# Kernel tuning notes

Measured on AMD Instinct MI355X. Metric: run time of the kernel, lower is better.

The kernel has to match this reference:

```python
import jax, jax.numpy as jnp
import numpy as np

D_MODEL = 1024
NUM_HEADS = 16
D_K = D_MODEL // NUM_HEADS
ROPE_THETA = 10000.0


def apply_rope(x, pos):
    # x: [B, H, S, d_k], pos: [S] int
    half = x.shape[-1] // 2
    inv_freq = ROPE_THETA ** (-jnp.arange(half, dtype=jnp.float32) * 2.0 / x.shape[-1])
    ang = pos.astype(jnp.float32)[:, None] * inv_freq[None, :]  # [S, half]
    cos, sin = jnp.cos(ang), jnp.sin(ang)
    x1 = x[..., 0::2]
    x2 = x[..., 1::2]
    r1 = x1 * cos - x2 * sin
    r2 = x1 * sin + x2 * cos
    return jnp.stack([r1, r2], axis=-1).reshape(x.shape)


def setup_inputs() -> dict:
    key = jax.random.key(0)
    ks = jax.random.split(key, 5)
    B, S = 4, 2048
    scale = 1.0 / np.sqrt(D_MODEL)
    x = jax.random.normal(ks[0], (B, S, D_MODEL), dtype=jnp.float32)
    w_q = jax.random.normal(ks[1], (D_MODEL, D_MODEL), dtype=jnp.float32) * scale
    w_k = jax.random.normal(ks[2], (D_MODEL, D_MODEL), dtype=jnp.float32) * scale
    w_v = jax.random.normal(ks[3], (D_MODEL, D_MODEL), dtype=jnp.float32) * scale
    w_o = jax.random.normal(ks[4], (D_MODEL, D_MODEL), dtype=jnp.float32) * scale
    token_positions = jnp.arange(S, dtype=jnp.int32)
    return {"x": x, "w_q": w_q, "w_k": w_k, "w_v": w_v, "w_o": w_o, "token_positions": token_positions}


def reference(x, w_q, w_k, w_v, w_o, token_positions):
    B, S, _ = x.shape
    def proj(w):
        return (x @ w.T).reshape(B, S, NUM_HEADS, D_K).transpose(0, 2, 1, 3)  # [B,H,S,d_k]
    q, k, v = proj(w_q), proj(w_k), proj(w_v)
    q = apply_rope(q, token_positions)
    k = apply_rope(k, token_positions)
    logits = jnp.einsum('bhid,bhjd->bhij', q, k) / jnp.sqrt(jnp.float32(D_K))
    causal = jnp.tril(jnp.ones((S, S), dtype=bool))
    logits = jnp.where(causal[None, None], logits, -jnp.inf)
    weights = jax.nn.softmax(logits, axis=-1)
    attn = jnp.einsum('bhij,bhjd->bhid', weights, v)  # [B,H,S,d_k]
    attn = attn.transpose(0, 2, 1, 3).reshape(B, S, D_MODEL)
    return attn @ w_o.T
```

## Files before the change

kernel.cpp:

```cpp
#include <hip/hip_runtime.h>
#include <hip/hip_bf16.h>
#include <stdint.h>

#define DM   1024
#define SEQ  2048
#define BATCH 4
#define NH   16
#define DK   64
#define NTK  16

typedef __attribute__((ext_vector_type(8))) __bf16 bf16x8;
typedef __attribute__((ext_vector_type(4))) float f32x4;
typedef __attribute__((ext_vector_type(4))) unsigned short ushort4_t;
typedef __attribute__((ext_vector_type(4))) unsigned int uint4_t;

typedef __attribute__((address_space(1))) const unsigned int GU32;
typedef __attribute__((address_space(3))) unsigned int LU32;

__device__ inline void gl_lds16(const void* g, void* l) {
  __builtin_amdgcn_global_load_lds((GU32*)g, (LU32*)l, 16, 0, 0);
}

__device__ inline f32x4 mfma16(bf16x8 a, bf16x8 b, f32x4 c) {
  return __builtin_amdgcn_mfma_f32_16x16x32_bf16(a, b, c, 0, 0, 0);
}

__device__ inline unsigned short f2bf(float f) {
  unsigned u = __float_as_uint(f);
  u += 0x7fffu + ((u >> 16) & 1u);
  return (unsigned short)(u >> 16);
}

__device__ inline unsigned cvt_pk_bf16(float a, float b) {
  unsigned r;
  asm("v_cvt_pk_bf16_f32 %0, %1, %2" : "=v"(r) : "v"(a), "v"(b));
  return r;
}

__device__ inline float fexp2(float x) {
  float r;
  asm("v_exp_f32 %0, %1" : "=v"(r) : "v"(x));
  return r;
}

__device__ inline int swz_of(int r) { return ((r & 6) << 2) | ((r & 1) << 5); }
__device__ inline int bswz(int r) { return ((r & 6) << 3) | ((r & 1) << 6); }

__global__ void prep_kernel(const float* __restrict__ x,
                            const float* __restrict__ wq, const float* __restrict__ wk,
                            const float* __restrict__ wv, const float* __restrict__ wo,
                            const int* __restrict__ tp,
                            unsigned short* __restrict__ xbf,
                            unsigned short* __restrict__ wbf,
                            float2* __restrict__ tab)
{
  const int NX4 = (BATCH*SEQ*DM)/4;
  const int NW4 = (DM*DM)/4;
  int idx = blockIdx.x*256 + threadIdx.x;
  if (idx < NX4) {
    float4 v = ((const float4*)x)[idx];
    ushort4_t o; o[0]=f2bf(v.x); o[1]=f2bf(v.y); o[2]=f2bf(v.z); o[3]=f2bf(v.w);
    ((ushort4_t*)xbf)[idx] = o;
  } else if (idx < NX4 + 4*NW4) {
    int t = idx - NX4;
    int wsel = t >> 18;
    int off = t & (NW4-1);
    const float* src = (wsel==0) ? wq : (wsel==1) ? wk : (wsel==2) ? wv : wo;
    float4 v = ((const float4*)src)[off];
    ushort4_t o; o[0]=f2bf(v.x); o[1]=f2bf(v.y); o[2]=f2bf(v.z); o[3]=f2bf(v.w);
    ((ushort4_t*)wbf)[wsel*NW4 + off] = o;
  } else {
    int t = idx - NX4 - 4*NW4;
    if (t < SEQ*32) {
      int s = t >> 5, i = t & 31;
      float invf = exp2f(-(float)i * (13.287712379549449f/32.0f));
      float ang = (float)tp[s] * invf;
      float sn, cs; sincosf(ang, &sn, &cs);
      tab[t] = make_float2(cs, sn);
    }
  }
}

template<int MODE>
__global__ __launch_bounds__(256, 2)
void gemm_db(const unsigned short* __restrict__ A,
             const unsigned short* __restrict__ Wall,
             unsigned short* __restrict__ qbf,
             unsigned short* __restrict__ kbf,
             unsigned short* __restrict__ vt,
             float* __restrict__ ofp,
             const float2* __restrict__ tab)
{
  __shared__ __align__(16) char lds[65536];
  const int tid = threadIdx.x;
  const int bid = blockIdx.x;
  int sel, mt, nt;
  if (MODE == 0) {
    sel = bid >> 9;
    int r = bid & 511;
    int xcd = r & 7, idx = r >> 3;
    mt = xcd*8 + (idx >> 3);  nt = idx & 7;
  } else {
    sel = 3;
    int xcd = bid & 7, idx = bid >> 3;
    mt = xcd*8 + (idx >> 3);  nt = idx & 7;
  }
  const unsigned short* Bm = Wall + (size_t)sel*DM*DM;
  const int a0 = mt*128, b0r = nt*128;
  const int w = tid>>6, lane = tid&63, ln = lane&15, g = lane>>4;
  const int wm = (w>>1)*64, wn = (w&1)*64;

  const char* src[8];
  {
    int rr = tid >> 3;
    int c  = (tid & 7) * 8;
    #pragma unroll
    for (int i = 0; i < 4; ++i) {
      int r_ = i*32 + rr;
      int cs = c ^ swz_of(r_);
      src[i]   = (const char*)(A  + (size_t)(a0  + r_)*DM + cs);
      src[i+4] = (const char*)(Bm + (size_t)(b0r + r_)*DM + cs);
    }
  }

  int offA[4], offB[4];
  #pragma unroll
  for (int m = 0; m < 4; ++m) {
    int R  = wm + m*16 + ln;
    offA[m] = R*128 + ((g*8 ^ swz_of(R)) * 2);
    int Rb = wn + m*16 + ln;
    offB[m] = 16384 + Rb*128 + ((g*8 ^ swz_of(Rb)) * 2);
  }

  f32x4 acc[4][4];
  #pragma unroll
  for (int i=0;i<4;i++)
    #pragma unroll
    for (int j=0;j<4;j++) acc[i][j] = (f32x4){0.f,0.f,0.f,0.f};

  #pragma unroll
  for (int i = 0; i < 8; ++i) gl_lds16(src[i],       lds +         i*4096 + tid*16);
  #pragma unroll
  for (int i = 0; i < 8; ++i) gl_lds16(src[i] + 128, lds + 32768 + i*4096 + tid*16);

  for (int t = 0; t < NTK; ++t) {
    char* sb = lds + (t & 1) * 32768;
    if (t < NTK-1) asm volatile("s_waitcnt vmcnt(8)" ::: "memory");
    else           asm volatile("s_waitcnt vmcnt(0)" ::: "memory");
    __builtin_amdgcn_sched_barrier(0);
    __builtin_amdgcn_s_barrier();
    asm volatile("" ::: "memory");
    __builtin_amdgcn_sched_barrier(0);

    bf16x8 fa[4][2], fb[4][2];
    #pragma unroll
    for (int m = 0; m < 4; ++m) {
      fa[m][0] = *(const bf16x8*)(sb + offA[m]);
      fa[m][1] = *(const bf16x8*)(sb + (offA[m] ^ 64));
      fb[m][0] = *(const bf16x8*)(sb + offB[m]);
      fb[m][1] = *(const bf16x8*)(sb + (offB[m] ^ 64));
    }
    asm volatile("s_waitcnt lgkmcnt(0)" ::: "memory");
    __builtin_amdgcn_sched_barrier(0);
    __builtin_amdgcn_s_barrier();
    asm volatile("" ::: "memory");
    __builtin_amdgcn_sched_barrier(0);

    if (t + 2 < NTK) {
      const int kb = (t + 2) * 128;
      #pragma unroll
      for (int i = 0; i < 8; ++i)
        gl_lds16(src[i] + kb, sb + i*4096 + tid*16);
    }
    __builtin_amdgcn_s_setprio(1);
    #pragma unroll
    for (int h = 0; h < 2; ++h)
      #pragma unroll
      for (int m = 0; m < 4; ++m)
        #pragma unroll
        for (int n = 0; n < 4; ++n)
          acc[m][n] = mfma16(fa[m][h], fb[n][h], acc[m][n]);
    __builtin_amdgcn_s_setprio(0);
  }

  if (MODE == 1) {
    #pragma unroll
    for (int i=0;i<4;i++) {
      int m = a0 + wm + i*16 + g*4;
      #pragma unroll
      for (int jn=0;jn<4;jn++) {
        int n = b0r + wn + jn*16 + ln;
        #pragma unroll
        for (int j=0;j<4;j++)
          ofp[(size_t)(m+j)*DM + n] = acc[i][jn][j];
      }
    }
  } else if (sel == 2) {
    #pragma unroll
    for (int i=0;i<4;i++) {
      int m0 = a0 + wm + i*16 + g*4;
      int bb = m0>>11, s0 = m0&2047;
      #pragma unroll
      for (int jn=0;jn<4;jn++) {
        int n = b0r + wn + jn*16 + ln;
        int h = n>>6, d = n&63;
        ushort4_t o4;
        #pragma unroll
        for (int j=0;j<4;j++) o4[j] = f2bf(acc[i][jn][j]);
        *(ushort4_t*)&vt[(((size_t)bb*NH + h)*DK + d)*SEQ + s0] = o4;
      }
    }
  } else {
    unsigned short* dst = sel ? kbf : qbf;
    const float qs = sel ? 1.0f : 0.1803368802f;
    #pragma unroll
    for (int jn=0;jn<4;jn++) {
      int n = b0r + wn + jn*16 + ln;
      int h = n>>6, d = n&63, di = d>>1, par = d&1;
      #pragma unroll
      for (int i=0;i<4;i++) {
        #pragma unroll
        for (int j=0;j<4;j++) {
          int m = a0 + wm + i*16 + g*4 + j;
          int bb = m>>11, s = m&2047;
          float v = acc[i][jn][j];
          float pv = __shfl_xor(v, 1);
          float2 cssn = tab[s*32 + di];
          float r = par ? (v*cssn.x + pv*cssn.y) : (v*cssn.x - pv*cssn.y);
          dst[((size_t)(bb*NH + h)*SEQ + s)*DK + d] = f2bf(r*qs);
        }
      }
    }
  }
}

__global__ __launch_bounds__(128, 2)
void attn_fa(const unsigned short* __restrict__ qbf,
             const unsigned short* __restrict__ kbf,
             const unsigned short* __restrict__ vtg,
             unsigned short* __restrict__ attnbf)
{
  __shared__ __align__(16) char kv_lds[32768];
  __shared__ __align__(16) char pl_lds[4096];
  const int bh = blockIdx.x, pr = blockIdx.y;
  const int qbA = 31 - pr;
  const int NTa = qbA + 1;
  const int NTtot = 33;
  const int tid = threadIdx.x, w = tid>>6, lane = tid&63, ln = lane&15, g = lane>>4;
  const int bb = bh>>4, h = bh&15;

  uint4_t ov = {0x3F803F80u, 0x3F803F80u, 0x3F803F80u, 0x3F803F80u};
  const bf16x8 ones = *(bf16x8*)&ov;

  const int rr = tid >> 3;
  const int cb = (tid & 7) * 16;
  const char* ks[4]; const char* vs[4];
  #pragma unroll
  for (int i = 0; i < 4; ++i) {
    int row = rr + i*16;
    ks[i] = (const char*)(kbf + ((size_t)bh*SEQ + row)*DK) + (cb ^ bswz(row));
    vs[i] = (const char*)(vtg + ((size_t)bh*DK  + row)*SEQ) + (cb ^ bswz(row));
  }

  const int ok0 = (g*16) ^ bswz(ln);
  char* plw = pl_lds + w*2048 + ln*128;
  const int plswz = (ln & 7) << 4;

  #pragma unroll
  for (int i = 0; i < 4; ++i) {
    gl_lds16(ks[i], kv_lds + i*2048 + tid*16);
    gl_lds16(vs[i], kv_lds + 8192 + i*2048 + tid*16);
  }
  #pragma unroll
  for (int i = 0; i < 4; ++i) {
    gl_lds16(ks[i] + 8192, kv_lds + 16384 + i*2048 + tid*16);
    gl_lds16(vs[i] + 128,  kv_lds + 16384 + 8192 + i*2048 + tid*16);
  }

  int q0a = qbA*64 + w*32;
  int q0b = q0a + 16;
  const unsigned short* qrA = qbf + ((size_t)bh*SEQ + q0a + ln)*DK;
  const unsigned short* qrB = qbf + ((size_t)bh*SEQ + q0b + ln)*DK;
  bf16x8 qa0 = *(const bf16x8*)(qrA + g*8);
  bf16x8 qa1 = *(const bf16x8*)(qrA + 32 + g*8);
  bf16x8 qb0 = *(const bf16x8*)(qrB + g*8);
  bf16x8 qb1 = *(const bf16x8*)(qrB + 32 + g*8);

  f32x4 oA[4], oB[4], osA, osB;
  #pragma unroll
  for (int f=0;f<4;f++) { oA[f] = (f32x4){0,0,0,0}; oB[f] = (f32x4){0,0,0,0}; }
  osA = (f32x4){0,0,0,0}; osB = (f32x4){0,0,0,0};

  for (int u = 0; u < NTtot; ++u) {
    const int tloc  = (u < NTa) ? u : u - NTa;
    const int NTcur = (u < NTa) ? NTa : NTtot - NTa;
    char* sb = kv_lds + (u & 1) * 16384;
    if (u < NTtot-1) asm volatile("s_waitcnt vmcnt(8)" ::: "memory");
    else             asm volatile("s_waitcnt vmcnt(0)" ::: "memory");
    __builtin_amdgcn_sched_barrier(0);
    __builtin_amdgcn_s_barrier();
    asm volatile("" ::: "memory");
    __builtin_amdgcn_sched_barrier(0);

    bf16x8 kf[4][2], vfr[4][2];
    #pragma unroll
    for (int a=0;a<4;a++) {
      kf[a][0]  = *(const bf16x8*)(sb + a*2048 + (ok0 ^  0) + ln*128);
      kf[a][1]  = *(const bf16x8*)(sb + a*2048 + (ok0 ^ 64) + ln*128);
      vfr[a][0] = *(const bf16x8*)(sb + 8192 + a*2048 + (ok0 ^  0) + ln*128);
      vfr[a][1] = *(const bf16x8*)(sb + 8192 + a*2048 + (ok0 ^ 64) + ln*128);
    }
    asm volatile("s_waitcnt lgkmcnt(0)" ::: "memory");
    __builtin_amdgcn_sched_barrier(0);
    __builtin_amdgcn_s_barrier();
    asm volatile("" ::: "memory");
    __builtin_amdgcn_sched_barrier(0);

    if (u + 2 < NTtot) {
      const int t2 = (u + 2 < NTa) ? u + 2 : u + 2 - NTa;
      const size_t kO = (size_t)t2*8192, vO = (size_t)t2*128;
      #pragma unroll
      for (int i = 0; i < 4; ++i) {
        gl_lds16(ks[i] + kO, sb + i*2048 + tid*16);
        gl_lds16(vs[i] + vO, sb + 8192 + i*2048 + tid*16);
      }
    }

    if (u == NTa) {
      #pragma unroll
      for (int j=0;j<4;j++) {
        float liA = 1.0f / osA[j];
        float liB = 1.0f / osB[j];
        int sA = q0a + g*4 + j, sB = q0b + g*4 + j;
        #pragma unroll
        for (int f=0;f<4;f++) {
          attnbf[((size_t)bb*SEQ + sA)*DM + h*DK + f*16 + ln] = f2bf(oA[f][j]*liA);
          attnbf[((size_t)bb*SEQ + sB)*DM + h*DK + f*16 + ln] = f2bf(oB[f][j]*liB);
        }
      }
      q0a = pr*64 + w*32;
      q0b = q0a + 16;
      const unsigned short* qa = qbf + ((size_t)bh*SEQ + q0a + ln)*DK;
      const unsigned short* qb = qbf + ((size_t)bh*SEQ + q0b + ln)*DK;
      qa0 = *(const bf16x8*)(qa + g*8);
      qa1 = *(const bf16x8*)(qa + 32 + g*8);
      qb0 = *(const bf16x8*)(qb + g*8);
      qb1 = *(const bf16x8*)(qb + 32 + g*8);
      #pragma unroll
      for (int f=0;f<4;f++) { oA[f] = (f32x4){0,0,0,0}; oB[f] = (f32x4){0,0,0,0}; }
      osA = (f32x4){0,0,0,0}; osB = (f32x4){0,0,0,0};
    }

    f32x4 saA[4], saB[4];
    __builtin_amdgcn_s_setprio(1);
    #pragma unroll
    for (int kvf=0;kvf<4;kvf++) {
      f32x4 za = (f32x4){0,0,0,0};
      za = mfma16(kf[kvf][0], qa0, za);
      za = mfma16(kf[kvf][1], qa1, za);
      saA[kvf] = za;
      f32x4 zb = (f32x4){0,0,0,0};
      zb = mfma16(kf[kvf][0], qb0, zb);
      zb = mfma16(kf[kvf][1], qb1, zb);
      saB[kvf] = zb;
    }
    __builtin_amdgcn_s_setprio(0);

    const bool diag = (tloc == NTcur-1);

    {
      if (diag) {
        int thr = q0a + ln - tloc*64 - g*4;
        #pragma unroll
        for (int kvf=0;kvf<4;kvf++)
          #pragma unroll
          for (int j=0;j<4;j++)
            if (kvf*16 + j > thr) saA[kvf][j] = -1e30f;
      }
      #pragma unroll
      for (int kvf=0;kvf<4;kvf++) {
        float p0 = fexp2(saA[kvf][0]);
        float p1 = fexp2(saA[kvf][1]);
        float p2 = fexp2(saA[kvf][2]);
        float p3 = fexp2(saA[kvf][3]);
        uint2 pk;
        pk.x = cvt_pk_bf16(p0, p1);
        pk.y = cvt_pk_bf16(p2, p3);
        *(uint2*)(plw + ((kvf*32 + g*8) ^ plswz)) = pk;
      }
      asm volatile("s_waitcnt lgkmcnt(0)" ::: "memory");
      __builtin_amdgcn_sched_barrier(0);
      #pragma unroll
      for (int c=0;c<2;c++) {
        bf16x8 pfA = *(const bf16x8*)(plw + ((c*64 + g*16) ^ plswz));
        #pragma unroll
        for (int f=0;f<4;f++)
          oA[f] = mfma16(pfA, vfr[f][c], oA[f]);
        osA = mfma16(pfA, ones, osA);
      }
    }

    {
      if (diag) {
        int thr = q0b + ln - tloc*64 - g*4;
        #pragma unroll
        for (int kvf=0;kvf<4;kvf++)
          #pragma unroll
          for (int j=0;j<4;j++)
            if (kvf*16 + j > thr) saB[kvf][j] = -1e30f;
      }
      #pragma unroll
      for (int kvf=0;kvf<4;kvf++) {
        float p0 = fexp2(saB[kvf][0]);
        float p1 = fexp2(saB[kvf][1]);
        float p2 = fexp2(saB[kvf][2]);
        float p3 = fexp2(saB[kvf][3]);
        uint2 pk;
        pk.x = cvt_pk_bf16(p0, p1);
        pk.y = cvt_pk_bf16(p2, p3);
        *(uint2*)(plw + ((kvf*32 + g*8) ^ plswz)) = pk;
      }
      asm volatile("s_waitcnt lgkmcnt(0)" ::: "memory");
      __builtin_amdgcn_sched_barrier(0);
      __builtin_amdgcn_s_setprio(1);
      #pragma unroll
      for (int c=0;c<2;c++) {
        bf16x8 pfB = *(const bf16x8*)(plw + ((c*64 + g*16) ^ plswz));
        #pragma unroll
        for (int f=0;f<4;f++)
          oB[f] = mfma16(pfB, vfr[f][c], oB[f]);
        osB = mfma16(pfB, ones, osB);
      }
      __builtin_amdgcn_s_setprio(0);
    }
  }

  #pragma unroll
  for (int j=0;j<4;j++) {
    float liA = 1.0f / osA[j];
    float liB = 1.0f / osB[j];
    int sA = q0a + g*4 + j, sB = q0b + g*4 + j;
    #pragma unroll
    for (int f=0;f<4;f++) {
      attnbf[((size_t)bb*SEQ + sA)*DM + h*DK + f*16 + ln] = f2bf(oA[f][j]*liA);
      attnbf[((size_t)bb*SEQ + sB)*DM + h*DK + f*16 + ln] = f2bf(oB[f][j]*liB);
    }
  }
}

extern "C" void kernel_launch(void* const* d_in, const int* in_sizes, int n_in,
                              void* d_out, int out_size, void* d_ws, size_t ws_size,
                              hipStream_t stream)
{
  const float* x  = (const float*)d_in[0];
  const float* wq = (const float*)d_in[1];
  const float* wk = (const float*)d_in[2];
  const float* wv = (const float*)d_in[3];
  const float* wo = (const float*)d_in[4];
  const int*   tp = (const int*)d_in[5];

  const size_t XB = (size_t)BATCH*SEQ*DM*2;
  const size_t WB = (size_t)DM*DM*2;

  char* ws = (char*)d_ws;
  unsigned short* xbf = (unsigned short*)(ws);
  unsigned short* qbf = (unsigned short*)(ws + XB);
  unsigned short* kbf = (unsigned short*)(ws + 2*XB);
  unsigned short* vt  = (unsigned short*)(ws + 3*XB);
  unsigned short* abf = (unsigned short*)(ws + 4*XB);
  unsigned short* wbf = (unsigned short*)(ws + 5*XB);
  float2* tab = (float2*)(ws + 5*XB + 4*WB);

  prep_kernel<<<12544, 256, 0, stream>>>(x, wq, wk, wv, wo, tp, xbf, wbf, tab);

  gemm_db<0><<<1536, 256, 0, stream>>>(xbf, wbf, qbf, kbf, vt, nullptr, tab);
  attn_fa<<<dim3(64,16), 128, 0, stream>>>(qbf, kbf, vt, abf);
  gemm_db<1><<<512, 256, 0, stream>>>(abf, wbf, nullptr, nullptr, nullptr,
                                      (float*)d_out, nullptr);
}
```

Before: 162.9 us.

## Replace QKV projection GEMM with 256x256-tile, 8-wave pipelined kernel

The QKV projection moves from 128x128 tiles with 4 waves to a new kernel using 256x256 tiles, 512 threads and a 128KB LDS double buffer. Each k-step is split into four quarter-stage loads interleaved with MFMA sub-blocks, so global-to-LDS traffic overlaps compute and operand reuse per tile goes up. The costs are 384 blocks that may not fill all CUs evenly, heavy register pressure from 32 accumulators per thread, and lower occupancy. The output GEMM keeps the old kernel, cut down to its output-projection mode, and the barrier sequences are folded into macros.

```diff
diff --git a/kernel.cpp b/kernel.cpp
--- a/kernel.cpp
+++ b/kernel.cpp
@@ -45,6 +45,15 @@
 
 __device__ inline int swz_of(int r) { return ((r & 6) << 2) | ((r & 1) << 5); }
 __device__ inline int bswz(int r) { return ((r & 6) << 3) | ((r & 1) << 6); }
+
+#define BAR_SYNC() do { \
+  __builtin_amdgcn_sched_barrier(0); \
+  __builtin_amdgcn_s_barrier(); \
+  asm volatile("" ::: "memory"); \
+  __builtin_amdgcn_sched_barrier(0); } while(0)
+#define LGKM0() do { \
+  asm volatile("s_waitcnt lgkmcnt(0)" ::: "memory"); \
+  __builtin_amdgcn_sched_barrier(0); } while(0)
 
 __global__ void prep_kernel(const float* __restrict__ x,
                             const float* __restrict__ wq, const float* __restrict__ wk,
@@ -81,31 +90,188 @@
   }
 }
 
+__global__ __launch_bounds__(512, 2)
+void gemm8(const unsigned short* __restrict__ A,
+           const unsigned short* __restrict__ Wall,
+           unsigned short* __restrict__ qbf,
+           unsigned short* __restrict__ kbf,
+           unsigned short* __restrict__ vt,
+           const float2* __restrict__ tab)
+{
+  __shared__ __align__(16) char lds[131072];
+  const int tid = threadIdx.x;
+  const int bid = blockIdx.x;
+  const int sel = bid >> 7;
+  const int rb = bid & 127;
+  const int xcd = rb & 7, idx = rb >> 3;
+  const int mt = xcd*4 + (idx>>2), nt = idx & 3;
+  const unsigned short* Bw = Wall + (size_t)sel*DM*DM;
+  const int a0 = mt*256, b0 = nt*256;
+  const int w = tid>>6, lane = tid&63, ln = lane&15, g = lane>>4;
+  const int wm = (w>>2)*128, wn = (w&3)*64;
+
+  const int r0 = tid >> 3;
+  const int csw = ((tid & 7) * 16) ^ bswz(r0);
+  const char* pA = (const char*)A  + ((size_t)(a0 + r0))*2048 + csw;
+  const char* pB = (const char*)Bw + ((size_t)(b0 + r0))*2048 + csw;
+
+  auto stage = [&](int hh) {
+    int T = hh>>2, j = hh&3;
+    const char* s = ((j<2) ? pB : pA) + (size_t)(j&1)*262144 + (size_t)T*128;
+    char* d = lds + (T&1)*65536 + ((j<2) ? (32768 + j*16384) : ((j-2)*16384))
+              + tid*16;
+    gl_lds16(s,          d);
+    gl_lds16(s + 131072, d + 8192);
+  };
+
+  const int swz = bswz(ln);
+  const int arow = (wm + ln)*128;
+  const int brow = 32768 + (wn + ln)*128;
+
+  f32x4 acc[8][4];
+  #pragma unroll
+  for (int i=0;i<8;i++)
+    #pragma unroll
+    for (int j=0;j<4;j++) acc[i][j] = (f32x4){0.f,0.f,0.f,0.f};
+
+  #pragma unroll
+  for (int hh = 0; hh < 6; ++hh) stage(hh);
+  asm volatile("s_waitcnt vmcnt(4)" ::: "memory");
+  BAR_SYNC();
+
+  int hptr = 6;
+  for (int U = 0; U < 16; ++U) {
+    char* sb = lds + (U&1)*65536;
+    bf16x8 Afr[4][2], Bfr[4][2];
+
+    #pragma unroll
+    for (int mi=0;mi<4;++mi)
+      #pragma unroll
+      for (int kh=0;kh<2;++kh)
+        Afr[mi][kh] = *(const bf16x8*)(sb + arow + mi*2048 + (((kh<<6)|(g<<4)) ^ swz));
+    #pragma unroll
+    for (int nf=0;nf<2;++nf)
+      #pragma unroll
+      for (int kh=0;kh<2;++kh)
+        Bfr[nf][kh] = *(const bf16x8*)(sb + brow + nf*2048 + (((kh<<6)|(g<<4)) ^ swz));
+    if (hptr < 64) stage(hptr++);
+    BAR_SYNC();
+    LGKM0();
+    __builtin_amdgcn_s_setprio(1);
+    #pragma unroll
+    for (int mi=0;mi<4;++mi)
+      #pragma unroll
+      for (int nf=0;nf<2;++nf)
+        #pragma unroll
+        for (int kh=0;kh<2;++kh)
+          acc[mi][nf] = mfma16(Afr[mi][kh], Bfr[nf][kh], acc[mi][nf]);
+    __builtin_amdgcn_s_setprio(0);
+    BAR_SYNC();
+
+    #pragma unroll
+    for (int nf=2;nf<4;++nf)
+      #pragma unroll
+      for (int kh=0;kh<2;++kh)
+        Bfr[nf][kh] = *(const bf16x8*)(sb + brow + nf*2048 + (((kh<<6)|(g<<4)) ^ swz));
+    if (hptr < 64) stage(hptr++);
+    BAR_SYNC();
+    LGKM0();
+    __builtin_amdgcn_s_setprio(1);
+    #pragma unroll
+    for (int mi=0;mi<4;++mi)
+      #pragma unroll
+      for (int nf=2;nf<4;++nf)
+        #pragma unroll
+        for (int kh=0;kh<2;++kh)
+          acc[mi][nf] = mfma16(Afr[mi][kh], Bfr[nf][kh], acc[mi][nf]);
+    __builtin_amdgcn_s_setprio(0);
+    BAR_SYNC();
+
+    #pragma unroll
+    for (int mi=0;mi<4;++mi)
+      #pragma unroll
+      for (int kh=0;kh<2;++kh)
+        Afr[mi][kh] = *(const bf16x8*)(sb + arow + 8192 + mi*2048 + (((kh<<6)|(g<<4)) ^ swz));
+    if (hptr < 64) stage(hptr++);
+    BAR_SYNC();
+    LGKM0();
+    __builtin_amdgcn_s_setprio(1);
+    #pragma unroll
+    for (int mi=0;mi<4;++mi)
+      #pragma unroll
+      for (int nf=0;nf<2;++nf)
+        #pragma unroll
+        for (int kh=0;kh<2;++kh)
+          acc[4+mi][nf] = mfma16(Afr[mi][kh], Bfr[nf][kh], acc[4+mi][nf]);
+    __builtin_amdgcn_s_setprio(0);
+    BAR_SYNC();
+
+    if (hptr < 64) stage(hptr++);
+    __builtin_amdgcn_s_setprio(1);
+    #pragma unroll
+    for (int mi=0;mi<4;++mi)
+      #pragma unroll
+      for (int nf=2;nf<4;++nf)
+        #pragma unroll
+        for (int kh=0;kh<2;++kh)
+          acc[4+mi][nf] = mfma16(Afr[mi][kh], Bfr[nf][kh], acc[4+mi][nf]);
+    __builtin_amdgcn_s_setprio(0);
+    if (U < 14)       asm volatile("s_waitcnt vmcnt(4)" ::: "memory");
+    else if (U == 14) asm volatile("s_waitcnt vmcnt(0)" ::: "memory");
+    BAR_SYNC();
+  }
+
+  if (sel == 2) {
+    #pragma unroll
+    for (int mi=0;mi<8;++mi) {
+      int m0 = a0 + wm + mi*16 + g*4;
+      int bb = m0>>11, s0 = m0&2047;
+      #pragma unroll
+      for (int nf=0;nf<4;++nf) {
+        int n = b0 + wn + nf*16 + ln;
+        int h = n>>6, d = n&63;
+        ushort4_t o4;
+        #pragma unroll
+        for (int jj=0;jj<4;++jj) o4[jj] = f2bf(acc[mi][nf][jj]);
+        *(ushort4_t*)&vt[(((size_t)bb*NH + h)*DK + d)*SEQ + s0] = o4;
+      }
+    }
+  } else {
+    unsigned short* dst = sel ? kbf : qbf;
+    const float qs = sel ? 1.0f : 0.1803368802f;
+    #pragma unroll
+    for (int nf=0;nf<4;++nf) {
+      int n = b0 + wn + nf*16 + ln;
+      int h = n>>6, d = n&63, di = d>>1, par = d&1;
+      #pragma unroll
+      for (int mi=0;mi<8;++mi) {
+        #pragma unroll
+        for (int jj=0;jj<4;++jj) {
+          int m = a0 + wm + mi*16 + g*4 + jj;
+          int bb = m>>11, s = m&2047;
+          float v = acc[mi][nf][jj];
+          float pv = __shfl_xor(v, 1);
+          float2 cssn = tab[s*32 + di];
+          float r = par ? (v*cssn.x + pv*cssn.y) : (v*cssn.x - pv*cssn.y);
+          dst[((size_t)(bb*NH + h)*SEQ + s)*DK + d] = f2bf(r*qs);
+        }
+      }
+    }
+  }
+}
+
 template<int MODE>
 __global__ __launch_bounds__(256, 2)
 void gemm_db(const unsigned short* __restrict__ A,
              const unsigned short* __restrict__ Wall,
-             unsigned short* __restrict__ qbf,
-             unsigned short* __restrict__ kbf,
-             unsigned short* __restrict__ vt,
-             float* __restrict__ ofp,
-             const float2* __restrict__ tab)
+             float* __restrict__ ofp)
 {
   __shared__ __align__(16) char lds[65536];
   const int tid = threadIdx.x;
   const int bid = blockIdx.x;
-  int sel, mt, nt;
-  if (MODE == 0) {
-    sel = bid >> 9;
-    int r = bid & 511;
-    int xcd = r & 7, idx = r >> 3;
-    mt = xcd*8 + (idx >> 3);  nt = idx & 7;
-  } else {
-    sel = 3;
-    int xcd = bid & 7, idx = bid >> 3;
-    mt = xcd*8 + (idx >> 3);  nt = idx & 7;
-  }
-  const unsigned short* Bm = Wall + (size_t)sel*DM*DM;
+  int xcd = bid & 7, idx = bid >> 3;
+  int mt = xcd*8 + (idx >> 3), nt = idx & 7;
+  const unsigned short* Bm = Wall + (size_t)3*DM*DM;
   const int a0 = mt*128, b0r = nt*128;
   const int w = tid>>6, lane = tid&63, ln = lane&15, g = lane>>4;
   const int wm = (w>>1)*64, wn = (w&1)*64;
@@ -147,10 +313,7 @@
     char* sb = lds + (t & 1) * 32768;
     if (t < NTK-1) asm volatile("s_waitcnt vmcnt(8)" ::: "memory");
     else           asm volatile("s_waitcnt vmcnt(0)" ::: "memory");
-    __builtin_amdgcn_sched_barrier(0);
-    __builtin_amdgcn_s_barrier();
-    asm volatile("" ::: "memory");
-    __builtin_amdgcn_sched_barrier(0);
+    BAR_SYNC();
 
     bf16x8 fa[4][2], fb[4][2];
     #pragma unroll
@@ -160,11 +323,8 @@
       fb[m][0] = *(const bf16x8*)(sb + offB[m]);
       fb[m][1] = *(const bf16x8*)(sb + (offB[m] ^ 64));
     }
-    asm volatile("s_waitcnt lgkmcnt(0)" ::: "memory");
-    __builtin_amdgcn_sched_barrier(0);
-    __builtin_amdgcn_s_barrier();
-    asm volatile("" ::: "memory");
-    __builtin_amdgcn_sched_barrier(0);
+    LGKM0();
+    BAR_SYNC();
 
     if (t + 2 < NTK) {
       const int kb = (t + 2) * 128;
@@ -183,53 +343,15 @@
     __builtin_amdgcn_s_setprio(0);
   }
 
-  if (MODE == 1) {
-    #pragma unroll
-    for (int i=0;i<4;i++) {
-      int m = a0 + wm + i*16 + g*4;
-      #pragma unroll
-      for (int jn=0;jn<4;jn++) {
-        int n = b0r + wn + jn*16 + ln;
-        #pragma unroll
-        for (int j=0;j<4;j++)
-          ofp[(size_t)(m+j)*DM + n] = acc[i][jn][j];
-      }
-    }
-  } else if (sel == 2) {
-    #pragma unroll
-    for (int i=0;i<4;i++) {
-      int m0 = a0 + wm + i*16 + g*4;
-      int bb = m0>>11, s0 = m0&2047;
-      #pragma unroll
-      for (int jn=0;jn<4;jn++) {
-        int n = b0r + wn + jn*16 + ln;
-        int h = n>>6, d = n&63;
-        ushort4_t o4;
-        #pragma unroll
-        for (int j=0;j<4;j++) o4[j] = f2bf(acc[i][jn][j]);
-        *(ushort4_t*)&vt[(((size_t)bb*NH + h)*DK + d)*SEQ + s0] = o4;
-      }
-    }
-  } else {
-    unsigned short* dst = sel ? kbf : qbf;
-    const float qs = sel ? 1.0f : 0.1803368802f;
+  #pragma unroll
+  for (int i=0;i<4;i++) {
+    int m = a0 + wm + i*16 + g*4;
     #pragma unroll
     for (int jn=0;jn<4;jn++) {
       int n = b0r + wn + jn*16 + ln;
-      int h = n>>6, d = n&63, di = d>>1, par = d&1;
-      #pragma unroll
-      for (int i=0;i<4;i++) {
-        #pragma unroll
-        for (int j=0;j<4;j++) {
-          int m = a0 + wm + i*16 + g*4 + j;
-          int bb = m>>11, s = m&2047;
-          float v = acc[i][jn][j];
-          float pv = __shfl_xor(v, 1);
-          float2 cssn = tab[s*32 + di];
-          float r = par ? (v*cssn.x + pv*cssn.y) : (v*cssn.x - pv*cssn.y);
-          dst[((size_t)(bb*NH + h)*SEQ + s)*DK + d] = f2bf(r*qs);
-        }
-      }
+      #pragma unroll
+      for (int j=0;j<4;j++)
+        ofp[(size_t)(m+j)*DM + n] = acc[i][jn][j];
     }
   }
 }
@@ -297,10 +419,7 @@
     char* sb = kv_lds + (u & 1) * 16384;
     if (u < NTtot-1) asm volatile("s_waitcnt vmcnt(8)" ::: "memory");
     else             asm volatile("s_waitcnt vmcnt(0)" ::: "memory");
-    __builtin_amdgcn_sched_barrier(0);
-    __builtin_amdgcn_s_barrier();
-    asm volatile("" ::: "memory");
-    __builtin_amdgcn_sched_barrier(0);
+    BAR_SYNC();
 
     bf16x8 kf[4][2], vfr[4][2];
     #pragma unroll
@@ -310,11 +429,8 @@
       vfr[a][0] = *(const bf16x8*)(sb + 8192 + a*2048 + (ok0 ^  0) + ln*128);
       vfr[a][1] = *(const bf16x8*)(sb + 8192 + a*2048 + (ok0 ^ 64) + ln*128);
     }
-    asm volatile("s_waitcnt lgkmcnt(0)" ::: "memory");
-    __builtin_amdgcn_sched_barrier(0);
-    __builtin_amdgcn_s_barrier();
-    asm volatile("" ::: "memory");
-    __builtin_amdgcn_sched_barrier(0);
+    LGKM0();
+    BAR_SYNC();
 
     if (u + 2 < NTtot) {
       const int t2 = (u + 2 < NTa) ? u + 2 : u + 2 - NTa;
@@ -473,8 +589,7 @@
 
   prep_kernel<<<12544, 256, 0, stream>>>(x, wq, wk, wv, wo, tp, xbf, wbf, tab);
 
-  gemm_db<0><<<1536, 256, 0, stream>>>(xbf, wbf, qbf, kbf, vt, nullptr, tab);
+  gemm8<<<384, 512, 0, stream>>>(xbf, wbf, qbf, kbf, vt, tab);
   attn_fa<<<dim3(64,16), 128, 0, stream>>>(qbf, kbf, vt, abf);
-  gemm_db<1><<<512, 256, 0, stream>>>(abf, wbf, nullptr, nullptr, nullptr,
-                                      (float*)d_out, nullptr);
-}
+  gemm_db<1><<<512, 256, 0, stream>>>(abf, wbf, (float*)d_out);
+}
```

Result: slower. 186.5 us (+14.5%).

## Split QKV GEMM into a K=32 tile variant with smaller LDS footprint

Applied to the files above, without the earlier changes.

The QKV projection GEMM becomes its own kernel that stages 32-wide K tiles (64 bytes per row) in 32KB of double-buffered LDS, using 32 iterations instead of 16. The output projection keeps the original 64-wide swizzled kernel. This is meant to reduce LDS use and allow more resident blocks, but it drops the XOR swizzle, which may cause bank conflicts. It also doubles the barrier count per unit of MFMA work.

```diff
diff --git a/kernel.cpp b/kernel.cpp
--- a/kernel.cpp
+++ b/kernel.cpp
@@ -8,6 +8,7 @@
 #define NH   16
 #define DK   64
 #define NTK  16
+#define NT32 32
 
 typedef __attribute__((ext_vector_type(8))) __bf16 bf16x8;
 typedef __attribute__((ext_vector_type(4))) float f32x4;
@@ -45,6 +46,15 @@
 
 __device__ inline int swz_of(int r) { return ((r & 6) << 2) | ((r & 1) << 5); }
 __device__ inline int bswz(int r) { return ((r & 6) << 3) | ((r & 1) << 6); }
+
+#define BAR_SYNC() do { \
+  __builtin_amdgcn_sched_barrier(0); \
+  __builtin_amdgcn_s_barrier(); \
+  asm volatile("" ::: "memory"); \
+  __builtin_amdgcn_sched_barrier(0); } while(0)
+#define LGKM0() do { \
+  asm volatile("s_waitcnt lgkmcnt(0)" ::: "memory"); \
+  __builtin_amdgcn_sched_barrier(0); } while(0)
 
 __global__ void prep_kernel(const float* __restrict__ x,
                             const float* __restrict__ wq, const float* __restrict__ wk,
@@ -81,121 +91,90 @@
   }
 }
 
-template<int MODE>
 __global__ __launch_bounds__(256, 2)
-void gemm_db(const unsigned short* __restrict__ A,
-             const unsigned short* __restrict__ Wall,
-             unsigned short* __restrict__ qbf,
-             unsigned short* __restrict__ kbf,
-             unsigned short* __restrict__ vt,
-             float* __restrict__ ofp,
-             const float2* __restrict__ tab)
+void gemm_qkv32(const unsigned short* __restrict__ A,
+                const unsigned short* __restrict__ Wall,
+                unsigned short* __restrict__ qbf,
+                unsigned short* __restrict__ kbf,
+                unsigned short* __restrict__ vt,
+                const float2* __restrict__ tab)
 {
-  __shared__ __align__(16) char lds[65536];
+  __shared__ __align__(16) char lds[32768];
   const int tid = threadIdx.x;
   const int bid = blockIdx.x;
-  int sel, mt, nt;
-  if (MODE == 0) {
-    sel = bid >> 9;
-    int r = bid & 511;
-    int xcd = r & 7, idx = r >> 3;
-    mt = xcd*8 + (idx >> 3);  nt = idx & 7;
-  } else {
-    sel = 3;
-    int xcd = bid & 7, idx = bid >> 3;
-    mt = xcd*8 + (idx >> 3);  nt = idx & 7;
-  }
+  const int sel = bid >> 9;
+  const int r = bid & 511;
+  const int xcd = r & 7, idx = r >> 3;
+  const int mt = xcd*8 + (idx >> 3), nt = idx & 7;
   const unsigned short* Bm = Wall + (size_t)sel*DM*DM;
   const int a0 = mt*128, b0r = nt*128;
   const int w = tid>>6, lane = tid&63, ln = lane&15, g = lane>>4;
   const int wm = (w>>1)*64, wn = (w&1)*64;
 
-  const char* src[8];
+  const int rr = tid >> 2;
+  const int cbyte = (tid & 3) * 16;
+  const char* aS0 = (const char*)(A  + (size_t)(a0 + rr)*DM) + cbyte;
+  const char* aS1 = (const char*)(A  + (size_t)(a0 + 64 + rr)*DM) + cbyte;
+  const char* bS0 = (const char*)(Bm + (size_t)(b0r + rr)*DM) + cbyte;
+  const char* bS1 = (const char*)(Bm + (size_t)(b0r + 64 + rr)*DM) + cbyte;
+  const int d0 = rr*64 + cbyte;
+
+  int offA[4], offB[4];
+  #pragma unroll
+  for (int m = 0; m < 4; ++m) {
+    offA[m] = (wm + m*16 + ln)*64 + g*16;
+    offB[m] = 8192 + (wn + m*16 + ln)*64 + g*16;
+  }
+
+  f32x4 acc[4][4];
+  #pragma unroll
+  for (int i=0;i<4;i++)
+    #pragma unroll
+    for (int j=0;j<4;j++) acc[i][j] = (f32x4){0.f,0.f,0.f,0.f};
+
   {
-    int rr = tid >> 3;
-    int c  = (tid & 7) * 8;
-    #pragma unroll
-    for (int i = 0; i < 4; ++i) {
-      int r_ = i*32 + rr;
-      int cs = c ^ swz_of(r_);
-      src[i]   = (const char*)(A  + (size_t)(a0  + r_)*DM + cs);
-      src[i+4] = (const char*)(Bm + (size_t)(b0r + r_)*DM + cs);
-    }
-  }
-
-  int offA[4], offB[4];
-  #pragma unroll
-  for (int m = 0; m < 4; ++m) {
-    int R  = wm + m*16 + ln;
-    offA[m] = R*128 + ((g*8 ^ swz_of(R)) * 2);
-    int Rb = wn + m*16 + ln;
-    offB[m] = 16384 + Rb*128 + ((g*8 ^ swz_of(Rb)) * 2);
-  }
-
-  f32x4 acc[4][4];
-  #pragma unroll
-  for (int i=0;i<4;i++)
-    #pragma unroll
-    for (int j=0;j<4;j++) acc[i][j] = (f32x4){0.f,0.f,0.f,0.f};
-
-  #pragma unroll
-  for (int i = 0; i < 8; ++i) gl_lds16(src[i],       lds +         i*4096 + tid*16);
-  #pragma unroll
-  for (int i = 0; i < 8; ++i) gl_lds16(src[i] + 128, lds + 32768 + i*4096 + tid*16);
-
-  for (int t = 0; t < NTK; ++t) {
-    char* sb = lds + (t & 1) * 32768;
-    if (t < NTK-1) asm volatile("s_waitcnt vmcnt(8)" ::: "memory");
-    else           asm volatile("s_waitcnt vmcnt(0)" ::: "memory");
-    __builtin_amdgcn_sched_barrier(0);
-    __builtin_amdgcn_s_barrier();
-    asm volatile("" ::: "memory");
-    __builtin_amdgcn_sched_barrier(0);
-
-    bf16x8 fa[4][2], fb[4][2];
+    gl_lds16(aS0,      lds +         d0);
+    gl_lds16(aS1,      lds +  4096 + d0);
+    gl_lds16(bS0,      lds +  8192 + d0);
+    gl_lds16(bS1,      lds + 12288 + d0);
+    gl_lds16(aS0 + 64, lds + 16384 +         d0);
+    gl_lds16(aS1 + 64, lds + 16384 +  4096 + d0);
+    gl_lds16(bS0 + 64, lds + 16384 +  8192 + d0);
+    gl_lds16(bS1 + 64, lds + 16384 + 12288 + d0);
+  }
+
+  for (int t = 0; t < NT32; ++t) {
+    char* sb = lds + (t & 1) * 16384;
+    if (t < NT32-1) asm volatile("s_waitcnt vmcnt(4)" ::: "memory");
+    else            asm volatile("s_waitcnt vmcnt(0)" ::: "memory");
+    BAR_SYNC();
+
+    bf16x8 fa[4], fb[4];
     #pragma unroll
     for (int m = 0; m < 4; ++m) {
-      fa[m][0] = *(const bf16x8*)(sb + offA[m]);
-      fa[m][1] = *(const bf16x8*)(sb + (offA[m] ^ 64));
-      fb[m][0] = *(const bf16x8*)(sb + offB[m]);
-      fb[m][1] = *(const bf16x8*)(sb + (offB[m] ^ 64));
-    }
-    asm volatile("s_waitcnt lgkmcnt(0)" ::: "memory");
-    __builtin_amdgcn_sched_barrier(0);
-    __builtin_amdgcn_s_barrier();
-    asm volatile("" ::: "memory");
-    __builtin_amdgcn_sched_barrier(0);
-
-    if (t + 2 < NTK) {
-      const int kb = (t + 2) * 128;
-      #pragma unroll
-      for (int i = 0; i < 8; ++i)
-        gl_lds16(src[i] + kb, sb + i*4096 + tid*16);
+      fa[m] = *(const bf16x8*)(sb + offA[m]);
+      fb[m] = *(const bf16x8*)(sb + offB[m]);
+    }
+    LGKM0();
+    BAR_SYNC();
+
+    if (t + 2 < NT32) {
+      const size_t kB = (size_t)(t + 2) * 64;
+      gl_lds16(aS0 + kB, sb +         d0);
+      gl_lds16(aS1 + kB, sb +  4096 + d0);
+      gl_lds16(bS0 + kB, sb +  8192 + d0);
+      gl_lds16(bS1 + kB, sb + 12288 + d0);
     }
     __builtin_amdgcn_s_setprio(1);
     #pragma unroll
-    for (int h = 0; h < 2; ++h)
-      #pragma unroll
-      for (int m = 0; m < 4; ++m)
-        #pragma unroll
-        for (int n = 0; n < 4; ++n)
-          acc[m][n] = mfma16(fa[m][h], fb[n][h], acc[m][n]);
+    for (int m = 0; m < 4; ++m)
+      #pragma unroll
+      for (int n = 0; n < 4; ++n)
+        acc[m][n] = mfma16(fa[m], fb[n], acc[m][n]);
     __builtin_amdgcn_s_setprio(0);
   }
 
-  if (MODE == 1) {
-    #pragma unroll
-    for (int i=0;i<4;i++) {
-      int m = a0 + wm + i*16 + g*4;
-      #pragma unroll
-      for (int jn=0;jn<4;jn++) {
-        int n = b0r + wn + jn*16 + ln;
-        #pragma unroll
-        for (int j=0;j<4;j++)
-          ofp[(size_t)(m+j)*DM + n] = acc[i][jn][j];
-      }
-    }
-  } else if (sel == 2) {
+  if (sel == 2) {
     #pragma unroll
     for (int i=0;i<4;i++) {
       int m0 = a0 + wm + i*16 + g*4;
@@ -226,10 +205,105 @@
           float v = acc[i][jn][j];
           float pv = __shfl_xor(v, 1);
           float2 cssn = tab[s*32 + di];
-          float r = par ? (v*cssn.x + pv*cssn.y) : (v*cssn.x - pv*cssn.y);
-          dst[((size_t)(bb*NH + h)*SEQ + s)*DK + d] = f2bf(r*qs);
+          float rr2 = par ? (v*cssn.x + pv*cssn.y) : (v*cssn.x - pv*cssn.y);
+          dst[((size_t)(bb*NH + h)*SEQ + s)*DK + d] = f2bf(rr2*qs);
         }
       }
+    }
+  }
+}
+
+__global__ __launch_bounds__(256, 2)
+void gemm_ot(const unsigned short* __restrict__ A,
+             const unsigned short* __restrict__ Wall,
+             float* __restrict__ ofp)
+{
+  __shared__ __align__(16) char lds[65536];
+  const int tid = threadIdx.x;
+  const int bid = blockIdx.x;
+  int xcd = bid & 7, idx = bid >> 3;
+  int mt = xcd*8 + (idx >> 3), nt = idx & 7;
+  const unsigned short* Bm = Wall + (size_t)3*DM*DM;
+  const int a0 = mt*128, b0r = nt*128;
+  const int w = tid>>6, lane = tid&63, ln = lane&15, g = lane>>4;
+  const int wm = (w>>1)*64, wn = (w&1)*64;
+
+  const char* src[8];
+  {
+    int rr = tid >> 3;
+    int c  = (tid & 7) * 8;
+    #pragma unroll
+    for (int i = 0; i < 4; ++i) {
+      int r_ = i*32 + rr;
+      int cs = c ^ swz_of(r_);
+      src[i]   = (const char*)(A  + (size_t)(a0  + r_)*DM + cs);
+      src[i+4] = (const char*)(Bm + (size_t)(b0r + r_)*DM + cs);
+    }
+  }
+
+  int offA[4], offB[4];
+  #pragma unroll
+  for (int m = 0; m < 4; ++m) {
+    int R  = wm + m*16 + ln;
+    offA[m] = R*128 + ((g*8 ^ swz_of(R)) * 2);
+    int Rb = wn + m*16 + ln;
+    offB[m] = 16384 + Rb*128 + ((g*8 ^ swz_of(Rb)) * 2);
+  }
+
+  f32x4 acc[4][4];
+  #pragma unroll
+  for (int i=0;i<4;i++)
+    #pragma unroll
+    for (int j=0;j<4;j++) acc[i][j] = (f32x4){0.f,0.f,0.f,0.f};
+
+  #pragma unroll
+  for (int i = 0; i < 8; ++i) gl_lds16(src[i],       lds +         i*4096 + tid*16);
+  #pragma unroll
+  for (int i = 0; i < 8; ++i) gl_lds16(src[i] + 128, lds + 32768 + i*4096 + tid*16);
+
+  for (int t = 0; t < NTK; ++t) {
+    char* sb = lds + (t & 1) * 32768;
+    if (t < NTK-1) asm volatile("s_waitcnt vmcnt(8)" ::: "memory");
+    else           asm volatile("s_waitcnt vmcnt(0)" ::: "memory");
+    BAR_SYNC();
+
+    bf16x8 fa[4][2], fb[4][2];
+    #pragma unroll
+    for (int m = 0; m < 4; ++m) {
+      fa[m][0] = *(const bf16x8*)(sb + offA[m]);
+      fa[m][1] = *(const bf16x8*)(sb + (offA[m] ^ 64));
+      fb[m][0] = *(const bf16x8*)(sb + offB[m]);
+      fb[m][1] = *(const bf16x8*)(sb + (offB[m] ^ 64));
+    }
+    LGKM0();
+    BAR_SYNC();
+
+    if (t + 2 < NTK) {
+      const int kb = (t + 2) * 128;
+      #pragma unroll
+      for (int i = 0; i < 8; ++i)
+        gl_lds16(src[i] + kb, sb + i*4096 + tid*16);
+    }
+    __builtin_amdgcn_s_setprio(1);
+    #pragma unroll
+    for (int h = 0; h < 2; ++h)
+      #pragma unroll
+      for (int m = 0; m < 4; ++m)
+        #pragma unroll
+        for (int n = 0; n < 4; ++n)
+          acc[m][n] = mfma16(fa[m][h], fb[n][h], acc[m][n]);
+    __builtin_amdgcn_s_setprio(0);
+  }
+
+  #pragma unroll
+  for (int i=0;i<4;i++) {
+    int m = a0 + wm + i*16 + g*4;
+    #pragma unroll
+    for (int jn=0;jn<4;jn++) {
+      int n = b0r + wn + jn*16 + ln;
+      #pragma unroll
+      for (int j=0;j<4;j++)
+        ofp[(size_t)(m+j)*DM + n] = acc[i][jn][j];
     }
   }
 }
@@ -297,10 +371,7 @@
     char* sb = kv_lds + (u & 1) * 16384;
     if (u < NTtot-1) asm volatile("s_waitcnt vmcnt(8)" ::: "memory");
     else             asm volatile("s_waitcnt vmcnt(0)" ::: "memory");
-    __builtin_amdgcn_sched_barrier(0);
-    __builtin_amdgcn_s_barrier();
-    asm volatile("" ::: "memory");
-    __builtin_amdgcn_sched_barrier(0);
+    BAR_SYNC();
 
     bf16x8 kf[4][2], vfr[4][2];
     #pragma unroll
@@ -310,11 +381,8 @@
       vfr[a][0] = *(const bf16x8*)(sb + 8192 + a*2048 + (ok0 ^  0) + ln*128);
       vfr[a][1] = *(const bf16x8*)(sb + 8192 + a*2048 + (ok0 ^ 64) + ln*128);
     }
-    asm volatile("s_waitcnt lgkmcnt(0)" ::: "memory");
-    __builtin_amdgcn_sched_barrier(0);
-    __builtin_amdgcn_s_barrier();
-    asm volatile("" ::: "memory");
-    __builtin_amdgcn_sched_barrier(0);
+    LGKM0();
+    BAR_SYNC();
 
     if (u + 2 < NTtot) {
       const int t2 = (u + 2 < NTa) ? u + 2 : u + 2 - NTa;
@@ -473,8 +541,7 @@
 
   prep_kernel<<<12544, 256, 0, stream>>>(x, wq, wk, wv, wo, tp, xbf, wbf, tab);
 
-  gemm_db<0><<<1536, 256, 0, stream>>>(xbf, wbf, qbf, kbf, vt, nullptr, tab);
+  gemm_qkv32<<<1536, 256, 0, stream>>>(xbf, wbf, qbf, kbf, vt, tab);
   attn_fa<<<dim3(64,16), 128, 0, stream>>>(qbf, kbf, vt, abf);
-  gemm_db<1><<<512, 256, 0, stream>>>(abf, wbf, nullptr, nullptr, nullptr,
-                                      (float*)d_out, nullptr);
-}
+  gemm_ot<<<512, 256, 0, stream>>>(abf, wbf, (float*)d_out);
+}
```

After: 169.4 us. 1.04x slower.
